# Performance work log

Measured on AMD Instinct MI355X. Metric: run time of the kernel, lower is better.

## Reference

```python
import jax, jax.numpy as jnp
import numpy as np

B, N, D, H, K, L, BLOCKS = 8, 256, 768, 12, 128, 4, 2
HD = D // H
SCALING = HD ** -0.5
NEG = -1e9  # stand-in for -inf; exp underflows to exactly 0 in softmax


def layernorm(x, s, b):
    m = x.mean(-1, keepdims=True)
    v = ((x - m) ** 2).mean(-1, keepdims=True)
    return (x - m) * jax.lax.rsqrt(v + 1e-5) * s + b


def _gauss(x, mean, std):
    a = (2.0 * 3.14159) ** 0.5
    return jnp.exp(-0.5 * ((x - mean) / std) ** 2) / (a * std)


def setup_inputs() -> dict:
    key = jax.random.key(0)
    ks = jax.random.split(key, 16)
    nrm = lambda k, shape: jax.random.normal(k, shape, jnp.float32) * 0.02
    atoms = jax.random.randint(ks[0], (B, N), 0, 10, dtype=jnp.int32)
    pos = jax.random.normal(ks[1], (B, N, 3), jnp.float32)
    atom_emb = nrm(ks[2], (10, D)).at[0].set(0.0)  # padding_idx=0
    gbf_means = jax.random.uniform(ks[3], (K,), jnp.float32, 0.0, 3.0)
    gbf_stds = jax.random.uniform(ks[4], (K,), jnp.float32, 0.0, 3.0)
    gbf_mul = jnp.ones((100, 1), jnp.float32)
    gbf_bias = jnp.zeros((100, 1), jnp.float32)
    bp_w1 = nrm(ks[5], (K, K)); bp_b1 = jnp.zeros((K,), jnp.float32)
    bp_w2 = nrm(ks[6], (K, H)); bp_b2 = jnp.zeros((H,), jnp.float32)
    edge_w = nrm(ks[7], (K, D)); edge_b = jnp.zeros((D,), jnp.float32)
    ap_w = nrm(ks[8], (D, D)); ap_b = jnp.zeros((D,), jnp.float32)
    ln1_s = jnp.ones((L, D), jnp.float32); ln1_b = jnp.zeros((L, D), jnp.float32)
    wi = nrm(ks[9], (L, D, 3 * D)); bi = jnp.zeros((L, 3 * D), jnp.float32)
    wo = nrm(ks[10], (L, D, D)); bo = jnp.zeros((L, D), jnp.float32)
    ln2_s = jnp.ones((L, D), jnp.float32); ln2_b = jnp.zeros((L, D), jnp.float32)
    w1 = nrm(ks[11], (L, D, D)); b1 = jnp.zeros((L, D), jnp.float32)
    w2 = nrm(ks[12], (L, D, D)); b2 = jnp.zeros((L, D), jnp.float32)
    fln_s = jnp.ones((D,), jnp.float32); fln_b = jnp.zeros((D,), jnp.float32)
    return dict(atoms=atoms, pos=pos, atom_emb=atom_emb, gbf_means=gbf_means,
                gbf_stds=gbf_stds, gbf_mul=gbf_mul, gbf_bias=gbf_bias,
                bp_w1=bp_w1, bp_b1=bp_b1, bp_w2=bp_w2, bp_b2=bp_b2,
                edge_w=edge_w, edge_b=edge_b, ap_w=ap_w, ap_b=ap_b,
                ln1_s=ln1_s, ln1_b=ln1_b, wi=wi, bi=bi, wo=wo, bo=bo,
                ln2_s=ln2_s, ln2_b=ln2_b, w1=w1, b1=b1, w2=w2, b2=b2,
                fln_s=fln_s, fln_b=fln_b)


def reference(atoms, pos, atom_emb, gbf_means, gbf_stds, gbf_mul, gbf_bias,
              bp_w1, bp_b1, bp_w2, bp_b2, edge_w, edge_b, ap_w, ap_b,
              ln1_s, ln1_b, wi, bi, wo, bo, ln2_s, ln2_b, w1, b1, w2, b2,
              fln_s, fln_b):
    pad = atoms == 0  # [B,N]
    delta = pos[:, None, :, :] - pos[:, :, None, :]  # [B,N,N,3]
    sq = (delta * delta).sum(-1)
    dist = jnp.where(sq > 0, jnp.sqrt(jnp.where(sq > 0, sq, 1.0)), 0.0)  # safe sqrt
    et = atoms[:, :, None] * 10 + atoms[:, None, :]  # [B,N,N] in [0,100)
    e = gbf_mul[et] * dist[..., None] + gbf_bias[et]  # [B,N,N,1]
    gbf = _gauss(e, gbf_means, jnp.abs(gbf_stds) + 1e-5)  # [B,N,N,K]
    # zero out padded j-columns, sum over j -> per-node edge feature
    ef = jnp.where(pad[:, None, :, None], 0.0, gbf).sum(axis=2)  # [B,N,K]
    node = atom_emb[atoms] + ef @ edge_w + edge_b  # [B,N,D]
    x = jnp.swapaxes(node, 0, 1) @ ap_w + ap_b  # [N,B,D]
    # attention bias: K-dim Gaussian features -> per-head bias
    bias = jax.nn.gelu(gbf @ bp_w1 + bp_b1, approximate=False) @ bp_w2 + bp_b2  # [B,N,N,H]
    bias = jnp.transpose(bias, (0, 3, 1, 2))  # [B,H,N,N]
    bias = jnp.where(pad[:, None, None, :], NEG, bias)

    def body(x, p):
        s1, c1, Wi, Bi, Wo, Bo, s2, c2, W1, B1, W2, B2 = p
        h = layernorm(x, s1, c1)
        q, k, v = jnp.split(h @ Wi + Bi, 3, axis=-1)
        q = q.reshape(N, B, H, HD) * SCALING
        k = k.reshape(N, B, H, HD)
        v = v.reshape(N, B, H, HD)
        sc = jnp.einsum('ibhd,jbhd->bhij', q, k) + bias
        pA = jax.nn.softmax(sc, axis=-1)
        o = jnp.einsum('bhij,jbhd->ibhd', pA, v).reshape(N, B, D)
        x = x + o @ Wo + Bo
        h = layernorm(x, s2, c2)
        h = jax.nn.gelu(h @ W1 + B1, approximate=False) @ W2 + B2
        return x + h, None

    stacked = (ln1_s, ln1_b, wi, bi, wo, bo, ln2_s, ln2_b, w1, b1, w2, b2)
    for _ in range(BLOCKS):
        x, _ = jax.lax.scan(body, x, stacked)
    x = layernorm(x, fln_s, fln_b)
    return jnp.swapaxes(x, 0, 1)  # [B,N,D]
```

## Files before the change

### kernel.cpp

```cpp
#include <hip/hip_runtime.h>
#include <math.h>

constexpr int Bn = 8, Nn = 256, Dn = 768, Hn = 12, Kn = 128;
constexpr int Tn = Nn * Bn;
constexpr float SCALE = 0.125f;
constexpr float NEGB = -1e9f;
constexpr float INV768 = 1.0f / 768.0f;

typedef __attribute__((ext_vector_type(8))) short bf16x8;
typedef __attribute__((ext_vector_type(4))) float f32x4;

#define MFMA16(a, b, c) __builtin_amdgcn_mfma_f32_16x16x32_bf16((a), (b), (c), 0, 0, 0)

__device__ __forceinline__ void gload_lds16(const void* g, void* l) {
  __builtin_amdgcn_global_load_lds(
      (const __attribute__((address_space(1))) void*)g,
      (__attribute__((address_space(3))) void*)l, 16, 0, 0);
}

__device__ __forceinline__ ushort f2bf(float x) {
  union { float f; unsigned u; } v; v.f = x;
  unsigned r = (v.u + 0x7fff + ((v.u >> 16) & 1)) >> 16;
  return (ushort)r;
}
__device__ __forceinline__ ushort f2bf_t(float x) {
  union { float f; unsigned u; } v; v.f = x;
  return (ushort)(v.u >> 16);
}
__device__ __forceinline__ float bf2f(ushort u) {
  union { unsigned u; float f; } v; v.u = ((unsigned)u) << 16;
  return v.f;
}
__device__ __forceinline__ unsigned pk2(float a, float b) {
  return (unsigned)f2bf_t(a) | ((unsigned)f2bf_t(b) << 16);
}
__device__ __forceinline__ float gelu_fast(float x) {
  float u = x * (0.7978845608f + 0.0356774081f * x * x);
  float e = __expf(2.0f * u);
  float t = 1.0f - 2.0f / (e + 1.0f);
  return 0.5f * x * (1.0f + t);
}
__device__ __forceinline__ float wave_sum(float v) {
#pragma unroll
  for (int off = 32; off; off >>= 1) v += __shfl_xor(v, off);
  return v;
}

__global__ __launch_bounds__(256) void wtrans_all(
    const float* __restrict__ ap_w, const float* __restrict__ wi,
    const float* __restrict__ wo, const float* __restrict__ w1,
    const float* __restrict__ w2, const float* __restrict__ bp_w1,
    const float* __restrict__ edge_w, const float* __restrict__ bp_w2,
    ushort* __restrict__ apT, ushort* __restrict__ wiT, ushort* __restrict__ woT,
    ushort* __restrict__ w1T, ushort* __restrict__ w2T, ushort* __restrict__ w1bT,
    ushort* __restrict__ ewT, ushort* __restrict__ w2b) {
  __shared__ float tile[64][65];
  int bid = blockIdx.x;
  int tid = threadIdx.x;
  const float* W; ushort* WT; int Kd, Nd, nx;
  if (bid < 144) { W = ap_w; WT = apT; Kd = 768; Nd = 768; nx = 12; }
  else if ((bid -= 144) < 1728) {
    int z = bid / 432; bid %= 432;
    W = wi + (size_t)z * 768 * 2304; WT = wiT + (size_t)z * 768 * 2304;
    Kd = 768; Nd = 2304; nx = 36;
  }
  else if ((bid -= 1728) < 576) {
    int z = bid / 144; bid %= 144;
    W = wo + (size_t)z * 768 * 768; WT = woT + (size_t)z * 768 * 768;
    Kd = 768; Nd = 768; nx = 12;
  }
  else if ((bid -= 576) < 576) {
    int z = bid / 144; bid %= 144;
    W = w1 + (size_t)z * 768 * 768; WT = w1T + (size_t)z * 768 * 768;
    Kd = 768; Nd = 768; nx = 12;
  }
  else if ((bid -= 576) < 576) {
    int z = bid / 144; bid %= 144;
    W = w2 + (size_t)z * 768 * 768; WT = w2T + (size_t)z * 768 * 768;
    Kd = 768; Nd = 768; nx = 12;
  }
  else if ((bid -= 576) < 4) { W = bp_w1; WT = w1bT; Kd = 128; Nd = 128; nx = 2; }
  else if ((bid -= 4) < 24) { W = edge_w; WT = ewT; Kd = 128; Nd = 768; nx = 12; }
  else {
    for (int e = tid; e < 2048; e += 256) {
      int h = e >> 7, k = e & 127;
      w2b[e] = (h < 12) ? f2bf(bp_w2[k * 12 + h]) : (ushort)0;
    }
    return;
  }
  int n0 = (bid % nx) * 64, k0 = (bid / nx) * 64;
  for (int e = tid; e < 64 * 64; e += 256) {
    int r = e >> 6, c = e & 63;
    tile[r][c] = W[(size_t)(k0 + r) * Nd + n0 + c];
  }
  __syncthreads();
  for (int e = tid; e < 64 * 64; e += 256) {
    int r = e >> 6, c = e & 63;
    WT[(size_t)(n0 + r) * Kd + k0 + c] = f2bf(tile[c][r]);
  }
}

__global__ __launch_bounds__(256) void gbias_kernel(
    const int* __restrict__ atoms, const float* __restrict__ pos,
    const float* __restrict__ means, const float* __restrict__ stds,
    const float* __restrict__ gmul, const float* __restrict__ gbias_,
    const ushort* __restrict__ w1T, const float* __restrict__ b1,
    const ushort* __restrict__ w2b, const float* __restrict__ b2,
    ushort* __restrict__ biasb, ushort* __restrict__ efb) {
  int i = blockIdx.x, b = blockIdx.y;
  __shared__ char W1s[32768];
  __shared__ char Ag[16384];
  __shared__ float sj[256];
  __shared__ int pml[256];
  __shared__ float b1s[128];
  const int tid = threadIdx.x, w = tid >> 6, ln = tid & 63;
  const int frow = ln & 15, fgrp = ln >> 4;
  {
    int srow = ln >> 4, sc = ln & 15;
#pragma unroll
    for (int q = 0; q < 8; ++q) {
      int inst = w * 8 + q;
      int row = inst * 4 + srow;
      const char* g = (const char*)(w1T + row * 128) + ((sc * 16) ^ ((row & 7) << 4));
      gload_lds16(g, W1s + inst * 1024);
    }
  }
  if (tid < 128) b1s[tid] = b1[tid];
  {
    int ai = atoms[b * Nn + i];
    int j = tid;
    int aj = atoms[b * Nn + j];
    float dx = pos[(b * Nn + i) * 3]     - pos[(b * Nn + j) * 3];
    float dy = pos[(b * Nn + i) * 3 + 1] - pos[(b * Nn + j) * 3 + 1];
    float dz = pos[(b * Nn + i) * 3 + 2] - pos[(b * Nn + j) * 3 + 2];
    float sq = dx * dx + dy * dy + dz * dz;
    float d = sq > 0.f ? sqrtf(sq) : 0.f;
    int et = ai * 10 + aj;
    sj[j] = fmaf(gmul[et], d, gbias_[et]);
    pml[j] = (aj == 0);
  }
  const int kp = tid & 63, rquad = tid >> 6;
  const int k0i = 2 * kp, k1i = 2 * kp + 1;
  float A0, B0, C0, cn0, A1, B1, C1, cn1;
  {
    float m0 = means[k0i], m1 = means[k1i];
    float sd0 = fabsf(stds[k0i]) + 1e-5f, sd1 = fabsf(stds[k1i]) + 1e-5f;
    float i0 = 1.0f / sd0, i1 = 1.0f / sd1;
    A0 = -0.5f * i0 * i0; B0 = -2.0f * A0 * m0; C0 = A0 * m0 * m0; cn0 = i0 * 0.3989423f;
    A1 = -0.5f * i1 * i1; B1 = -2.0f * A1 * m1; C1 = A1 * m1 * m1; cn1 = i1 * 0.3989423f;
  }
  __syncthreads();
  float facc0 = 0.f, facc1 = 0.f;

  for (int jt = 0; jt < 4; ++jt) {
    int j0 = jt * 64;
#pragma unroll
    for (int rr = 0; rr < 16; ++rr) {
      int row = rquad * 16 + rr;
      int jg = j0 + row;
      float s = sj[jg];
      float e0 = __expf(fmaf(fmaf(A0, s, B0), s, C0));
      float e1 = __expf(fmaf(fmaf(A1, s, B1), s, C1));
      int padj = pml[jg];
      facc0 += padj ? 0.f : e0;
      facc1 += padj ? 0.f : e1;
      *(unsigned*)(Ag + row * 256 + ((4 * kp) ^ ((row & 7) << 4))) = pk2(e0 * cn0, e1 * cn1);
    }
    f32x4 acc[8] = {};
    const int arow = w * 16 + frow;
#pragma unroll
    for (int ks = 0; ks < 4; ++ks) {
      bf16x8 af = *(const bf16x8*)(Ag + arow * 256 + ((ks * 64 + fgrp * 16) ^ ((arow & 7) << 4)));
#pragma unroll
      for (int nt = 0; nt < 8; ++nt) {
        int brow = nt * 16 + frow;
        bf16x8 bfv = *(const bf16x8*)(W1s + brow * 256 + ((ks * 64 + fgrp * 16) ^ ((brow & 7) << 4)));
        acc[nt] = MFMA16(af, bfv, acc[nt]);
      }
    }
#pragma unroll
    for (int nt = 0; nt < 8; ++nt) {
      int n = nt * 16 + frow;
#pragma unroll
      for (int r = 0; r < 4; ++r) {
        int jloc = w * 16 + fgrp * 4 + r;
        float g = gelu_fast(acc[nt][r] + b1s[n]);
        *(ushort*)(Ag + jloc * 256 + ((2 * n) ^ ((jloc & 7) << 4))) = f2bf_t(g);
      }
    }
    {
      f32x4 acc2 = {};
      int jrow = w * 16 + frow;
      const ushort* w2p = w2b + frow * 128;
#pragma unroll
      for (int ks = 0; ks < 4; ++ks) {
        bf16x8 af = *(const bf16x8*)(Ag + jrow * 256 + ((ks * 64 + fgrp * 16) ^ ((jrow & 7) << 4)));
        bf16x8 bfv = *(const bf16x8*)(w2p + ks * 32 + fgrp * 8);
        acc2 = MFMA16(af, bfv, acc2);
      }
      if (frow < 12) {
        float bv = b2[frow];
#pragma unroll
        for (int r = 0; r < 4; ++r) {
          int jl = w * 16 + fgrp * 4 + r;
          int jg = j0 + jl;
          float v = pml[jg] ? NEGB : (acc2[r] + bv);
          biasb[(((size_t)b * Hn + frow) * Nn + i) * Nn + jg] = f2bf(v);
        }
      }
    }
  }
  __syncthreads();
  {
    float* efp = (float*)Ag;
    efp[(kp * 4 + rquad) * 2 + 0] = facc0;
    efp[(kp * 4 + rquad) * 2 + 1] = facc1;
    __syncthreads();
    if (tid < 128) {
      int k = tid, kq = k >> 1, lo = k & 1;
      float s = efp[(kq * 4 + 0) * 2 + lo] + efp[(kq * 4 + 1) * 2 + lo] +
                efp[(kq * 4 + 2) * 2 + lo] + efp[(kq * 4 + 3) * 2 + lo];
      float cn = 0.3989423f / (fabsf(stds[k]) + 1e-5f);
      efb[(size_t)(b * Nn + i) * Kn + k] = f2bf(s * cn);
    }
  }
}

template <int MODE>
__global__ __launch_bounds__(256, 4) void mgemm(
    const ushort* __restrict__ A, const ushort* __restrict__ WT,
    const float* __restrict__ bias, const float* __restrict__ res,
    void* __restrict__ Cout, const int* __restrict__ atomsp,
    const float* __restrict__ embp, int M, int Kd, int Nd) {
  __shared__ char smem[32768];
  char* ldsA = smem;
  char* ldsB = smem + 16384;
  const int tid = threadIdx.x, w = tid >> 6, ln = tid & 63;
  const int m0 = blockIdx.y * 64, n0 = blockIdx.x * 64;
  const int wm = (w >> 1) * 32, wn = (w & 1) * 32;
  const int srow = ln >> 4, schunk = ln & 15;
  const int frow = ln & 15, fgrp = ln >> 4;
  f32x4 acc[2][2] = {};
  for (int kt = 0; kt < Kd; kt += 128) {
    __syncthreads();
#pragma unroll
    for (int q = 0; q < 4; ++q) {
      int I = w * 4 + q;
      int r = I * 4 + srow;
      gload_lds16((const char*)(A + (size_t)(m0 + r) * Kd + kt) +
                      ((schunk * 16) ^ ((r & 7) << 4)),
                  ldsA + I * 1024);
    }
#pragma unroll
    for (int q = 0; q < 4; ++q) {
      int I = w * 4 + q;
      int r = I * 4 + srow;
      gload_lds16((const char*)(WT + (size_t)(n0 + r) * Kd + kt) +
                      ((schunk * 16) ^ ((r & 7) << 4)),
                  ldsB + I * 1024);
    }
    __syncthreads();
#pragma unroll
    for (int ks = 0; ks < 4; ++ks) {
      bf16x8 af[2], bfv[2];
#pragma unroll
      for (int mt = 0; mt < 2; ++mt) {
        int row = wm + mt * 16 + frow;
        af[mt] = *(const bf16x8*)(ldsA + row * 256 + ((ks * 64 + fgrp * 16) ^ ((row & 7) << 4)));
      }
#pragma unroll
      for (int nt = 0; nt < 2; ++nt) {
        int row = wn + nt * 16 + frow;
        bfv[nt] = *(const bf16x8*)(ldsB + row * 256 + ((ks * 64 + fgrp * 16) ^ ((row & 7) << 4)));
      }
      acc[0][0] = MFMA16(af[0], bfv[0], acc[0][0]);
      acc[0][1] = MFMA16(af[0], bfv[1], acc[0][1]);
      acc[1][0] = MFMA16(af[1], bfv[0], acc[1][0]);
      acc[1][1] = MFMA16(af[1], bfv[1], acc[1][1]);
    }
  }
#pragma unroll
  for (int nt = 0; nt < 2; ++nt) {
    int n = n0 + wn + nt * 16 + frow;
    float bv = bias[n];
#pragma unroll
    for (int mt = 0; mt < 2; ++mt) {
#pragma unroll
      for (int r = 0; r < 4; ++r) {
        int m = m0 + wm + mt * 16 + fgrp * 4 + r;
        float v = acc[mt][nt][r] + bv;
        if (MODE == 1) v = gelu_fast(v);
        if (MODE == 2) v += res[(size_t)m * Nd + n];
        if (MODE == 5) v += embp[(size_t)atomsp[m] * Nd + n];
        if (MODE == 2 || MODE == 3) ((float*)Cout)[(size_t)m * Nd + n] = v;
        else                        ((ushort*)Cout)[(size_t)m * Nd + n] = f2bf(v);
      }
    }
  }
}

__global__ __launch_bounds__(256, 2) void mgemm128_qkv(
    const ushort* __restrict__ A, const ushort* __restrict__ WT,
    const float* __restrict__ bias, ushort* __restrict__ vTout,
    ushort* __restrict__ Cout, int M, int Kd, int Nd) {
  __shared__ char smem[32768];
  char* ldsA = smem;
  char* ldsB = smem + 16384;
  const int tid = threadIdx.x, w = tid >> 6, ln = tid & 63;
  const int m0 = blockIdx.y * 128, n0 = blockIdx.x * 128;
  const int wm = (w >> 1) * 64, wn = (w & 1) * 64;
  const int srow = ln >> 3, schunk = ln & 7;
  const int sswz = (schunk * 16) ^ (srow << 4);
  const int frow = ln & 15, fgrp = ln >> 4;
  f32x4 acc[4][4] = {};
  for (int kt = 0; kt < Kd; kt += 64) {
    __syncthreads();
#pragma unroll
    for (int q = 0; q < 4; ++q) {
      int r = (w * 4 + q) * 8 + srow;
      gload_lds16((const char*)(A + (size_t)(m0 + r) * Kd + kt) + sswz, ldsA + (w * 4 + q) * 1024);
    }
#pragma unroll
    for (int q = 0; q < 4; ++q) {
      int r = (w * 4 + q) * 8 + srow;
      gload_lds16((const char*)(WT + (size_t)(n0 + r) * Kd + kt) + sswz, ldsB + (w * 4 + q) * 1024);
    }
    __syncthreads();
#pragma unroll
    for (int ks = 0; ks < 2; ++ks) {
      bf16x8 af[4], bfv[4];
#pragma unroll
      for (int mt = 0; mt < 4; ++mt) {
        int row = wm + mt * 16 + frow;
        af[mt] = *(const bf16x8*)(ldsA + row * 128 + ((ks * 64 + fgrp * 16) ^ ((row & 7) << 4)));
      }
#pragma unroll
      for (int nt = 0; nt < 4; ++nt) {
        int row = wn + nt * 16 + frow;
        bfv[nt] = *(const bf16x8*)(ldsB + row * 128 + ((ks * 64 + fgrp * 16) ^ ((row & 7) << 4)));
      }
#pragma unroll
      for (int mt = 0; mt < 4; ++mt)
#pragma unroll
        for (int nt = 0; nt < 4; ++nt)
          acc[mt][nt] = MFMA16(af[mt], bfv[nt], acc[mt][nt]);
    }
  }
#pragma unroll
  for (int nt = 0; nt < 4; ++nt) {
    int n = n0 + wn + nt * 16 + frow;
    float bv = bias[n];
    if (n >= 1536) {
      int dd = n - 1536, h = dd >> 6, d = dd & 63;
#pragma unroll
      for (int mt = 0; mt < 4; ++mt) {
#pragma unroll
        for (int r = 0; r < 4; ++r) {
          int m = m0 + wm + mt * 16 + fgrp * 4 + r;
          int bb = m >> 8, j = m & 255;
          vTout[(((size_t)bb * Hn + h) * 64 + d) * 256 + j] = f2bf(acc[mt][nt][r] + bv);
        }
      }
    } else {
      float sc = (n < 768) ? SCALE : 1.0f;
#pragma unroll
      for (int mt = 0; mt < 4; ++mt) {
#pragma unroll
        for (int r = 0; r < 4; ++r) {
          int m = m0 + wm + mt * 16 + fgrp * 4 + r;
          Cout[(size_t)m * Nd + n] = f2bf((acc[mt][nt][r] + bv) * sc);
        }
      }
    }
  }
}

__global__ __launch_bounds__(256, 2) void attn_mfma(
    const ushort* __restrict__ qkv, const ushort* __restrict__ vT,
    const ushort* __restrict__ biasb, ushort* __restrict__ Oout) {
  int it = blockIdx.x, h = blockIdx.y, b = blockIdx.z;
  int i0 = it * 64;
  __shared__ char smem[65536];
  char* Ks = smem;
  char* Vs = smem + 32768;
  const int tid = threadIdx.x, w = tid >> 6, ln = tid & 63;
  const int frow = ln & 15, fgrp = ln >> 4;
  {
    const int srow = ln >> 3, schunk = ln & 7;
#pragma unroll
    for (int q = 0; q < 8; ++q) {
      int inst = w * 8 + q;
      int row = inst * 8 + srow;
      const char* g = (const char*)(qkv + (size_t)(b * Nn + row) * 2304 + 768 + h * 64) +
                      ((schunk * 16) ^ ((row & 7) << 4));
      gload_lds16(g, Ks + inst * 1024);
    }
#pragma unroll
    for (int q = 0; q < 8; ++q) {
      int inst = w * 8 + q;
      int row = inst * 2 + (ln >> 5);
      int cb = (ln & 31) * 16;
      const char* g = (const char*)(vT + (size_t)((b * Hn + h) * 64 + row) * 256) +
                      (cb ^ ((row & 7) << 4));
      gload_lds16(g, Vs + inst * 1024);
    }
  }
  bf16x8 qf[2];
  {
    int qrow = i0 + w * 16 + frow;
    const ushort* qg = qkv + (size_t)(b * Nn + qrow) * 2304 + h * 64 + fgrp * 8;
    qf[0] = *(const bf16x8*)qg;
    qf[1] = *(const bf16x8*)(qg + 32);
  }
  __syncthreads();
  f32x4 s[16];
#pragma unroll
  for (int jtl = 0; jtl < 16; ++jtl) {
    int row = jtl * 16 + frow;
    const char* kb = Ks + row * 128;
    bf16x8 k0 = *(const bf16x8*)(kb + ((fgrp * 16) ^ ((row & 7) << 4)));
    bf16x8 k1 = *(const bf16x8*)(kb + ((64 + fgrp * 16) ^ ((row & 7) << 4)));
    f32x4 t = {};
    t = MFMA16(qf[0], k0, t);
    t = MFMA16(qf[1], k1, t);
    s[jtl] = t;
  }
  float inv[4];
#pragma unroll
  for (int r = 0; r < 4; ++r) {
    int i = i0 + w * 16 + fgrp * 4 + r;
    const ushort* brow = biasb + (((size_t)b * Hn + h) * Nn + i) * Nn;
    float su = 0.f;
#pragma unroll
    for (int jtl = 0; jtl < 16; ++jtl) {
      float p = __expf(s[jtl][r] + bf2f(brow[jtl * 16 + frow]));
      s[jtl][r] = p;
      su += p;
    }
    su += __shfl_xor(su, 1); su += __shfl_xor(su, 2);
    su += __shfl_xor(su, 4); su += __shfl_xor(su, 8);
    inv[r] = 1.0f / su;
  }
  __syncthreads();
  char* Ps = Ks + w * 8192;
#pragma unroll
  for (int r = 0; r < 4; ++r) {
    int prow = fgrp * 4 + r;
#pragma unroll
    for (int jtl = 0; jtl < 16; ++jtl) {
      int cb = jtl * 32 + frow * 2;
      *(ushort*)(Ps + prow * 512 + (cb ^ ((prow & 7) << 4))) = f2bf_t(s[jtl][r]);
    }
  }
  __syncthreads();
  bf16x8 pf[8];
#pragma unroll
  for (int ks = 0; ks < 8; ++ks)
    pf[ks] = *(const bf16x8*)(Ps + frow * 512 + ((ks * 64 + fgrp * 16) ^ ((frow & 7) << 4)));
  f32x4 o[4] = {};
#pragma unroll
  for (int dt = 0; dt < 4; ++dt) {
#pragma unroll
    for (int ks = 0; ks < 8; ++ks) {
      int row = dt * 16 + frow;
      bf16x8 vf = *(const bf16x8*)(Vs + row * 512 + ((ks * 64 + fgrp * 16) ^ ((row & 7) << 4)));
      o[dt] = MFMA16(pf[ks], vf, o[dt]);
    }
  }
#pragma unroll
  for (int dt = 0; dt < 4; ++dt)
#pragma unroll
    for (int r = 0; r < 4; ++r) {
      int i = i0 + w * 16 + fgrp * 4 + r;
      Oout[(size_t)(b * Nn + i) * Dn + h * 64 + dt * 16 + frow] = f2bf(o[dt][r] * inv[r]);
    }
}

template <int MODE>
__global__ __launch_bounds__(256) void ln_kernel(
    const float* __restrict__ x, const float* __restrict__ sc,
    const float* __restrict__ bi, void* __restrict__ out) {
  int t = blockIdx.x;
  int tid = threadIdx.x;
  const float* xr = x + (size_t)t * Dn;
  float v0 = xr[tid], v1 = xr[tid + 256], v2 = xr[tid + 512];
  __shared__ float red[4], red2[4];
  float s = wave_sum(v0 + v1 + v2);
  if ((tid & 63) == 0) red[tid >> 6] = s;
  __syncthreads();
  float mean = (red[0] + red[1] + red[2] + red[3]) * INV768;
  float d0 = v0 - mean, d1 = v1 - mean, d2 = v2 - mean;
  float vs = wave_sum(d0 * d0 + d1 * d1 + d2 * d2);
  if ((tid & 63) == 0) red2[tid >> 6] = vs;
  __syncthreads();
  float var = (red2[0] + red2[1] + red2[2] + red2[3]) * INV768;
  float r = rsqrtf(var + 1e-5f);
  if (MODE == 0) {
    ushort* o = (ushort*)out + (size_t)t * Dn;
    o[tid]       = f2bf(d0 * r * sc[tid]       + bi[tid]);
    o[tid + 256] = f2bf(d1 * r * sc[tid + 256] + bi[tid + 256]);
    o[tid + 512] = f2bf(d2 * r * sc[tid + 512] + bi[tid + 512]);
  } else {
    float* o = (float*)out + (size_t)t * Dn;
    o[tid]       = d0 * r * sc[tid]       + bi[tid];
    o[tid + 256] = d1 * r * sc[tid + 256] + bi[tid + 256];
    o[tid + 512] = d2 * r * sc[tid + 512] + bi[tid + 512];
  }
}

extern "C" void kernel_launch(void* const* d_in, const int* in_sizes, int n_in,
                              void* d_out, int out_size, void* d_ws, size_t ws_size,
                              hipStream_t stream) {
  (void)in_sizes; (void)n_in; (void)out_size; (void)ws_size;
  const int*   atoms    = (const int*)  d_in[0];
  const float* pos      = (const float*)d_in[1];
  const float* atom_emb = (const float*)d_in[2];
  const float* gbf_means= (const float*)d_in[3];
  const float* gbf_stds = (const float*)d_in[4];
  const float* gbf_mul  = (const float*)d_in[5];
  const float* gbf_bias = (const float*)d_in[6];
  const float* bp_w1    = (const float*)d_in[7];
  const float* bp_b1    = (const float*)d_in[8];
  const float* bp_w2    = (const float*)d_in[9];
  const float* bp_b2    = (const float*)d_in[10];
  const float* edge_w   = (const float*)d_in[11];
  const float* edge_b   = (const float*)d_in[12];
  const float* ap_w     = (const float*)d_in[13];
  const float* ap_b     = (const float*)d_in[14];
  const float* ln1_s    = (const float*)d_in[15];
  const float* ln1_b    = (const float*)d_in[16];
  const float* wi       = (const float*)d_in[17];
  const float* bi       = (const float*)d_in[18];
  const float* wo       = (const float*)d_in[19];
  const float* bo       = (const float*)d_in[20];
  const float* ln2_s    = (const float*)d_in[21];
  const float* ln2_b    = (const float*)d_in[22];
  const float* w1       = (const float*)d_in[23];
  const float* b1       = (const float*)d_in[24];
  const float* w2       = (const float*)d_in[25];
  const float* b2       = (const float*)d_in[26];
  const float* fln_s    = (const float*)d_in[27];
  const float* fln_b    = (const float*)d_in[28];
  float* out = (float*)d_out;

  ushort* wsb   = (ushort*)d_ws;
  ushort* biasb = wsb;
  ushort* qkvb  = biasb + (size_t)Bn * Hn * Nn * Nn;
  ushort* hb    = qkvb + (size_t)Tn * 2304;
  ushort* vT    = hb + (size_t)Tn * Dn;
  ushort* wiT   = vT + (size_t)Bn * Hn * 64 * 256;
  ushort* woT   = wiT + (size_t)4 * 2304 * Dn;
  ushort* w1T   = woT + (size_t)4 * Dn * Dn;
  ushort* w2T   = w1T + (size_t)4 * Dn * Dn;
  ushort* w1bT  = w2T + (size_t)4 * Dn * Dn;
  ushort* w2b   = w1bT + 16384;
  float*  xbuf  = (float*)(w2b + 2048);
  ushort* apT   = qkvb;
  ushort* ewT   = qkvb + 589824;
  ushort* ffnb  = qkvb;
  ushort* efb   = vT;

  wtrans_all<<<3629, 256, 0, stream>>>(ap_w, wi, wo, w1, w2, bp_w1, edge_w, bp_w2,
                                       apT, wiT, woT, w1T, w2T, w1bT, ewT, w2b);

  dim3 gridNB(Nn, Bn);
  gbias_kernel<<<gridNB, 256, 0, stream>>>(atoms, pos, gbf_means, gbf_stds,
                                           gbf_mul, gbf_bias, w1bT, bp_b1, w2b, bp_b2,
                                           biasb, efb);
  mgemm<5><<<dim3(12, 32), 256, 0, stream>>>(efb, ewT, edge_b, nullptr, hb,
                                             atoms, atom_emb, Tn, 128, Dn);
  mgemm<3><<<dim3(12, 32), 256, 0, stream>>>(hb, apT, ap_b, nullptr, xbuf,
                                             nullptr, nullptr, Tn, Dn, Dn);

  for (int it = 0; it < 8; ++it) {
    int l = it & 3;
    ln_kernel<0><<<Tn, 256, 0, stream>>>(xbuf, ln1_s + l * Dn, ln1_b + l * Dn, hb);
    mgemm128_qkv<<<dim3(18, 16), 256, 0, stream>>>(hb, wiT + (size_t)l * 2304 * Dn,
                                                   bi + l * 2304, vT, qkvb, Tn, Dn, 2304);
    attn_mfma<<<dim3(4, Hn, Bn), 256, 0, stream>>>(qkvb, vT, biasb, hb);
    mgemm<2><<<dim3(12, 32), 256, 0, stream>>>(hb, woT + (size_t)l * Dn * Dn,
                                               bo + l * Dn, xbuf, xbuf,
                                               nullptr, nullptr, Tn, Dn, Dn);
    ln_kernel<0><<<Tn, 256, 0, stream>>>(xbuf, ln2_s + l * Dn, ln2_b + l * Dn, hb);
    mgemm<1><<<dim3(12, 32), 256, 0, stream>>>(hb, w1T + (size_t)l * Dn * Dn,
                                               b1 + l * Dn, nullptr, ffnb,
                                               nullptr, nullptr, Tn, Dn, Dn);
    mgemm<2><<<dim3(12, 32), 256, 0, stream>>>(ffnb, w2T + (size_t)l * Dn * Dn,
                                               b2 + l * Dn, xbuf, xbuf,
                                               nullptr, nullptr, Tn, Dn, Dn);
  }
  ln_kernel<1><<<Tn, 256, 0, stream>>>(xbuf, fln_s, fln_b, out);
}
```

Baseline: 668.9 us.

## Fold log2e into scores and bias, use raw exp2/rcp, permute bias for vector loads

Result: faster. 643.7 us (-3.8%).

```diff
diff --git a/kernel.cpp b/kernel.cpp
--- a/kernel.cpp
+++ b/kernel.cpp
@@ -4,6 +4,7 @@
 constexpr int Bn = 8, Nn = 256, Dn = 768, Hn = 12, Kn = 128;
 constexpr int Tn = Nn * Bn;
 constexpr float SCALE = 0.125f;
+constexpr float LOG2E = 1.4426950408889634f;
 constexpr float NEGB = -1e9f;
 constexpr float INV768 = 1.0f / 768.0f;
 
@@ -18,6 +19,13 @@
       (__attribute__((address_space(3))) void*)l, 16, 0, 0);
 }
 
+__device__ __forceinline__ float fexp2(float x) {
+  float r;
+  asm("v_exp_f32 %0, %1" : "=v"(r) : "v"(x));
+  return r;
+}
+__device__ __forceinline__ float frcp(float x) { return __builtin_amdgcn_rcpf(x); }
+
 __device__ __forceinline__ ushort f2bf(float x) {
   union { float f; unsigned u; } v; v.f = x;
   unsigned r = (v.u + 0x7fff + ((v.u >> 16) & 1)) >> 16;
@@ -36,9 +44,12 @@
 }
 __device__ __forceinline__ float gelu_fast(float x) {
   float u = x * (0.7978845608f + 0.0356774081f * x * x);
-  float e = __expf(2.0f * u);
-  float t = 1.0f - 2.0f / (e + 1.0f);
+  float e = fexp2(2.8853901f * u);
+  float t = 1.0f - 2.0f * frcp(e + 1.0f);
   return 0.5f * x * (1.0f + t);
+}
+__device__ __forceinline__ float gelu_sig(float x) {
+  return x * frcp(1.0f + fexp2(-2.4554669f * x));
 }
 __device__ __forceinline__ float wave_sum(float v) {
 #pragma unroll
@@ -146,8 +157,9 @@
     float m0 = means[k0i], m1 = means[k1i];
     float sd0 = fabsf(stds[k0i]) + 1e-5f, sd1 = fabsf(stds[k1i]) + 1e-5f;
     float i0 = 1.0f / sd0, i1 = 1.0f / sd1;
-    A0 = -0.5f * i0 * i0; B0 = -2.0f * A0 * m0; C0 = A0 * m0 * m0; cn0 = i0 * 0.3989423f;
-    A1 = -0.5f * i1 * i1; B1 = -2.0f * A1 * m1; C1 = A1 * m1 * m1; cn1 = i1 * 0.3989423f;
+    float a0 = -0.5f * i0 * i0 * LOG2E, a1 = -0.5f * i1 * i1 * LOG2E;
+    A0 = a0; B0 = -2.0f * a0 * m0; C0 = a0 * m0 * m0; cn0 = i0 * 0.3989423f;
+    A1 = a1; B1 = -2.0f * a1 * m1; C1 = a1 * m1 * m1; cn1 = i1 * 0.3989423f;
   }
   __syncthreads();
   float facc0 = 0.f, facc1 = 0.f;
@@ -159,8 +171,8 @@
       int row = rquad * 16 + rr;
       int jg = j0 + row;
       float s = sj[jg];
-      float e0 = __expf(fmaf(fmaf(A0, s, B0), s, C0));
-      float e1 = __expf(fmaf(fmaf(A1, s, B1), s, C1));
+      float e0 = fexp2(fmaf(fmaf(A0, s, B0), s, C0));
+      float e1 = fexp2(fmaf(fmaf(A1, s, B1), s, C1));
       int padj = pml[jg];
       facc0 += padj ? 0.f : e0;
       facc1 += padj ? 0.f : e1;
@@ -184,7 +196,7 @@
 #pragma unroll
       for (int r = 0; r < 4; ++r) {
         int jloc = w * 16 + fgrp * 4 + r;
-        float g = gelu_fast(acc[nt][r] + b1s[n]);
+        float g = gelu_sig(acc[nt][r] + b1s[n]);
         *(ushort*)(Ag + jloc * 256 + ((2 * n) ^ ((jloc & 7) << 4))) = f2bf_t(g);
       }
     }
@@ -204,8 +216,9 @@
         for (int r = 0; r < 4; ++r) {
           int jl = w * 16 + fgrp * 4 + r;
           int jg = j0 + jl;
-          float v = pml[jg] ? NEGB : (acc2[r] + bv);
-          biasb[(((size_t)b * Hn + frow) * Nn + i) * Nn + jg] = f2bf(v);
+          float v = pml[jg] ? NEGB : (acc2[r] + bv) * LOG2E;
+          int pj = ((jg & 15) << 4) | (jg >> 4);
+          biasb[(((size_t)b * Hn + frow) * Nn + i) * Nn + pj] = f2bf(v);
         }
       }
     }
@@ -362,7 +375,7 @@
         }
       }
     } else {
-      float sc = (n < 768) ? SCALE : 1.0f;
+      float sc = (n < 768) ? SCALE * LOG2E : 1.0f;
 #pragma unroll
       for (int mt = 0; mt < 4; ++mt) {
 #pragma unroll
@@ -429,17 +442,20 @@
 #pragma unroll
   for (int r = 0; r < 4; ++r) {
     int i = i0 + w * 16 + fgrp * 4 + r;
-    const ushort* brow = biasb + (((size_t)b * Hn + h) * Nn + i) * Nn;
+    const ushort* brow = biasb + (((size_t)b * Hn + h) * Nn + i) * Nn + frow * 16;
+    bf16x8 b0 = *(const bf16x8*)brow;
+    bf16x8 b1 = *(const bf16x8*)(brow + 8);
     float su = 0.f;
 #pragma unroll
     for (int jtl = 0; jtl < 16; ++jtl) {
-      float p = __expf(s[jtl][r] + bf2f(brow[jtl * 16 + frow]));
+      float bv = bf2f((ushort)(jtl < 8 ? b0[jtl] : b1[jtl - 8]));
+      float p = fexp2(s[jtl][r] + bv);
       s[jtl][r] = p;
       su += p;
     }
     su += __shfl_xor(su, 1); su += __shfl_xor(su, 2);
     su += __shfl_xor(su, 4); su += __shfl_xor(su, 8);
-    inv[r] = 1.0f / su;
+    inv[r] = frcp(su);
   }
   __syncthreads();
   char* Ps = Ks + w * 8192;
```
